# Performance work log

Hardware: AMD Instinct MI355X
Metric: run time of the kernel (lower is better)

Reference implementation:

```python
import jax, jax.numpy as jnp
import numpy as np
from jax import lax

EPS = 1e-06


def setup_inputs() -> dict:
    key = jax.random.key(0)
    B, MICS, T, F = 16, 4, 2048, 257
    x = jax.random.uniform(key, (B, MICS, T, F), dtype=jnp.float32)
    s = jnp.array([0.025], dtype=jnp.float32)
    alpha = jnp.array([0.98], dtype=jnp.float32)
    delta = jnp.array([2.0], dtype=jnp.float32)
    r = jnp.array([0.5], dtype=jnp.float32)
    return {"x": x, "s": s, "alpha": alpha, "delta": delta, "r": r}


def reference(x, s, alpha, delta, r):
    # x: [batch, mics, chans, frames]; EMA recurrence runs over dim 2 (split dim -2 in source)
    B, MICS, T, F = x.shape
    xr = x.reshape(B * MICS, T, F)
    xt = jnp.moveaxis(xr, 1, 0)  # [T, BM, F] -- scan axis first

    s0 = s[0]

    def step(carry, frame):
        m = (1.0 - s0) * carry + s0 * frame
        return m, m

    m0 = xt[0]  # first frame: M_0 = x_0 (last_state=None branch)
    _, ms = lax.scan(step, m0, xt[1:])
    M = jnp.concatenate([m0[None], ms], axis=0)  # [T, BM, F]
    M = jnp.moveaxis(M, 0, 1)  # [BM, T, F]

    # pcen nonlinearity: (x / (M+eps)^alpha + delta)^r - delta^r
    out = jnp.power(xr / jnp.power(M + EPS, alpha) + delta, r) - jnp.power(delta, r)
    return out.reshape(B, MICS, T, F)
```

## Files before the change

kernel.cpp:

```cpp
#include <hip/hip_runtime.h>
#include <hip/hip_bf16.h>


#define EPS 1e-6f

constexpr int BM = 64;
constexpr int T  = 2048;
constexpr int F  = 257;
constexpr int L  = 32;
constexpr int C  = T / L;
constexpr int NBLK = BM * C;
constexpr size_t MLOC_BYTES = (size_t)BM * C * F * sizeof(float);

__device__ __forceinline__ float fast_exp2(float x) { return __builtin_amdgcn_exp2f(x); }
__device__ __forceinline__ float fast_log2(float x) { return __builtin_amdgcn_logf(x); }

__device__ __forceinline__ float pcen_nl(float xv, float m, float alpha,
                                         float delta, float r, float dr) {
  float inner = fmaf(xv, fast_exp2(-alpha * fast_log2(m + EPS)), delta);
  return fast_exp2(r * fast_log2(inner)) - dr;
}

__global__ __launch_bounds__(64, 4) void pcen_phase1(
    const float* __restrict__ x, const float* __restrict__ s_p,
    float* __restrict__ mloc) {
  const int b  = blockIdx.x;
  const int l  = threadIdx.x;
  const int bm = b >> 6;
  const int c  = b & (C - 1);

  const float s = s_p[0];
  const float a = 1.0f - s;

  const float* row = x + ((size_t)bm * T + (size_t)c * L) * F;

  float m0, m1, m2, m3, m4;
  if (c == 0) {
    m0 = row[l]; m1 = row[l + 64]; m2 = row[l + 128]; m3 = row[l + 192];
    m4 = row[256];
  } else {
    m0 = m1 = m2 = m3 = m4 = 0.0f;
  }

  const float* p = row;
  #pragma unroll 4
  for (int t = 0; t < L; ++t) {
    float x0 = p[l];
    float x1 = p[l + 64];
    float x2 = p[l + 128];
    float x3 = p[l + 192];
    float x4 = p[256];
    m0 = fmaf(a, m0, s * x0);
    m1 = fmaf(a, m1, s * x1);
    m2 = fmaf(a, m2, s * x2);
    m3 = fmaf(a, m3, s * x3);
    m4 = fmaf(a, m4, s * x4);
    p += F;
  }

  float* mp = mloc + ((size_t)bm * C + c) * F;
  mp[l] = m0; mp[l + 64] = m1; mp[l + 128] = m2; mp[l + 192] = m3;
  if (l == 0) mp[256] = m4;
}

__global__ __launch_bounds__(64, 4) void pcen_phase2(
    const float* __restrict__ x, const float* __restrict__ s_p,
    const float* __restrict__ alpha_p, const float* __restrict__ delta_p,
    const float* __restrict__ r_p, const float* __restrict__ mloc,
    float* __restrict__ out) {
  const int b  = blockIdx.x;
  const int l  = threadIdx.x;
  const int bm = b >> 6;
  const int c  = b & (C - 1);

  const float s     = s_p[0];
  const float a     = 1.0f - s;
  const float alpha = alpha_p[0];
  const float delta = delta_p[0];
  const float r     = r_p[0];
  const float dr    = fast_exp2(r * fast_log2(delta));

  float aL = a;
  #pragma unroll
  for (int i = 0; i < 5; ++i) aL *= aL;

  const size_t rowoff = ((size_t)bm * T + (size_t)c * L) * F;
  const float* row  = x + rowoff;
  float*       orow = out + rowoff;

  float m0, m1, m2, m3, m4;
  if (c == 0) {
    m0 = row[l]; m1 = row[l + 64]; m2 = row[l + 128]; m3 = row[l + 192];
    m4 = row[256];
  } else {
    const float* mp = mloc + (size_t)bm * C * F;
    m0 = mp[l]; m1 = mp[l + 64]; m2 = mp[l + 128]; m3 = mp[l + 192];
    m4 = mp[256];
    const float* q = mp + F;
    #pragma unroll 2
    for (int cc = 1; cc < c; ++cc) {
      m0 = fmaf(aL, m0, q[l]);
      m1 = fmaf(aL, m1, q[l + 64]);
      m2 = fmaf(aL, m2, q[l + 128]);
      m3 = fmaf(aL, m3, q[l + 192]);
      m4 = fmaf(aL, m4, q[256]);
      q += F;
    }
  }

  const float* p  = row;
  float*       op = orow;
  #pragma unroll 2
  for (int t = 0; t < L; ++t) {
    float x0 = p[l];
    float x1 = p[l + 64];
    float x2 = p[l + 128];
    float x3 = p[l + 192];
    float x4 = p[256];
    m0 = fmaf(a, m0, s * x0);
    m1 = fmaf(a, m1, s * x1);
    m2 = fmaf(a, m2, s * x2);
    m3 = fmaf(a, m3, s * x3);
    m4 = fmaf(a, m4, s * x4);
    __builtin_nontemporal_store(pcen_nl(x0, m0, alpha, delta, r, dr), &op[l]);
    __builtin_nontemporal_store(pcen_nl(x1, m1, alpha, delta, r, dr), &op[l + 64]);
    __builtin_nontemporal_store(pcen_nl(x2, m2, alpha, delta, r, dr), &op[l + 128]);
    __builtin_nontemporal_store(pcen_nl(x3, m3, alpha, delta, r, dr), &op[l + 192]);
    if (l == 0)
      __builtin_nontemporal_store(pcen_nl(x4, m4, alpha, delta, r, dr), &op[256]);
    p  += F;
    op += F;
  }
}

constexpr int FB_L = 128;
constexpr int FB_C = T / FB_L;
constexpr int FB_H = 256;
__global__ __launch_bounds__(64, 4) void pcen_fallback(
    const float* __restrict__ x, const float* __restrict__ s_p,
    const float* __restrict__ alpha_p, const float* __restrict__ delta_p,
    const float* __restrict__ r_p, float* __restrict__ out) {
  const int b  = blockIdx.x;
  const int l  = threadIdx.x;
  const int bm = b / FB_C;
  const int c  = b % FB_C;

  const float s     = s_p[0];
  const float a     = 1.0f - s;
  const float alpha = alpha_p[0];
  const float delta = delta_p[0];
  const float r     = r_p[0];
  const float dr    = fast_exp2(r * fast_log2(delta));

  const size_t colbase = (size_t)bm * T * F;
  const int tstart = c * FB_L;
  int t0 = tstart - FB_H; if (t0 < 0) t0 = 0;

  float m0, m1, m2, m3, m4;
  const float* row0 = x + colbase + (size_t)t0 * F;
  if (t0 == 0) {
    m0 = row0[l]; m1 = row0[l + 64]; m2 = row0[l + 128]; m3 = row0[l + 192];
    m4 = row0[256];
  } else {
    m0 = m1 = m2 = m3 = m4 = 0.0f;
  }

  const float* p = row0;
  for (int t = t0; t < tstart; ++t) {
    float x0 = p[l], x1 = p[l + 64], x2 = p[l + 128], x3 = p[l + 192], x4 = p[256];
    m0 = fmaf(a, m0, s * x0); m1 = fmaf(a, m1, s * x1);
    m2 = fmaf(a, m2, s * x2); m3 = fmaf(a, m3, s * x3);
    m4 = fmaf(a, m4, s * x4);
    p += F;
  }
  p = x + colbase + (size_t)tstart * F;
  float* op = out + colbase + (size_t)tstart * F;
  for (int t = 0; t < FB_L; ++t) {
    float x0 = p[l], x1 = p[l + 64], x2 = p[l + 128], x3 = p[l + 192], x4 = p[256];
    m0 = fmaf(a, m0, s * x0); m1 = fmaf(a, m1, s * x1);
    m2 = fmaf(a, m2, s * x2); m3 = fmaf(a, m3, s * x3);
    m4 = fmaf(a, m4, s * x4);
    __builtin_nontemporal_store(pcen_nl(x0, m0, alpha, delta, r, dr), &op[l]);
    __builtin_nontemporal_store(pcen_nl(x1, m1, alpha, delta, r, dr), &op[l + 64]);
    __builtin_nontemporal_store(pcen_nl(x2, m2, alpha, delta, r, dr), &op[l + 128]);
    __builtin_nontemporal_store(pcen_nl(x3, m3, alpha, delta, r, dr), &op[l + 192]);
    if (l == 0)
      __builtin_nontemporal_store(pcen_nl(x4, m4, alpha, delta, r, dr), &op[256]);
    p  += F;
    op += F;
  }
}

extern "C" void kernel_launch(void* const* d_in, const int* in_sizes, int n_in,
                              void* d_out, int out_size, void* d_ws, size_t ws_size,
                              hipStream_t stream) {
  const float* x     = (const float*)d_in[0];
  const float* s     = (const float*)d_in[1];
  const float* alpha = (const float*)d_in[2];
  const float* delta = (const float*)d_in[3];
  const float* r     = (const float*)d_in[4];
  float* out = (float*)d_out;

  if (d_ws != nullptr && ws_size >= MLOC_BYTES) {
    float* mloc = (float*)d_ws;
    pcen_phase1<<<NBLK, 64, 0, stream>>>(x, s, mloc);
    pcen_phase2<<<NBLK, 64, 0, stream>>>(x, s, alpha, delta, r, mloc, out);
  } else {
    pcen_fallback<<<BM * FB_C, 64, 0, stream>>>(x, s, alpha, delta, r, out);
  }
}
```

Measured before the change: 301.0 us.

## Stage time tiles through double-buffered LDS with float4 loads, larger chunks

Both phases now use 256-thread blocks that copy contiguous 16-frame tiles of x into a double-buffered shared-memory buffer with coalesced float4 loads, then run the per-column EMA scan from LDS. Each thread owns one frequency column instead of five, and the chunk length grows from 32 to 128 frames, so there are fewer chunks and a shorter carry-prefix loop in phase 2. The goal is to replace strided scalar global loads with wide contiguous loads and overlap prefetch with compute. In exchange there are fewer blocks (1024), a barrier per tile, and a serial column 256 handled by a single thread.

```diff
diff --git a/kernel.cpp b/kernel.cpp
--- a/kernel.cpp
+++ b/kernel.cpp
@@ -1,5 +1,4 @@
 #include <hip/hip_runtime.h>
-#include <hip/hip_bf16.h>
 
 
 #define EPS 1e-6f
@@ -7,9 +6,12 @@
 constexpr int BM = 64;
 constexpr int T  = 2048;
 constexpr int F  = 257;
-constexpr int L  = 32;
+constexpr int L  = 128;
 constexpr int C  = T / L;
-constexpr int NBLK = BM * C;
+constexpr int TF = 16;
+constexpr int NT = L / TF;
+constexpr int NQ = TF * F / 4;
+constexpr int BLKS = BM * C;
 constexpr size_t MLOC_BYTES = (size_t)BM * C * F * sizeof(float);
 
 __device__ __forceinline__ float fast_exp2(float x) { return __builtin_amdgcn_exp2f(x); }
@@ -21,57 +23,81 @@
   return fast_exp2(r * fast_log2(inner)) - dr;
 }
 
-__global__ __launch_bounds__(64, 4) void pcen_phase1(
+__global__ __launch_bounds__(256, 4) void pcen_phase1(
     const float* __restrict__ x, const float* __restrict__ s_p,
     float* __restrict__ mloc) {
-  const int b  = blockIdx.x;
-  const int l  = threadIdx.x;
-  const int bm = b >> 6;
-  const int c  = b & (C - 1);
+  __shared__ float4 sb[2][NQ];
+  const int tid = threadIdx.x;
+  const int bm  = blockIdx.x >> 4;
+  const int c   = blockIdx.x & (C - 1);
 
   const float s = s_p[0];
   const float a = 1.0f - s;
 
-  const float* row = x + ((size_t)bm * T + (size_t)c * L) * F;
-
-  float m0, m1, m2, m3, m4;
-  if (c == 0) {
-    m0 = row[l]; m1 = row[l + 64]; m2 = row[l + 128]; m3 = row[l + 192];
-    m4 = row[256];
-  } else {
-    m0 = m1 = m2 = m3 = m4 = 0.0f;
-  }
-
-  const float* p = row;
-  #pragma unroll 4
-  for (int t = 0; t < L; ++t) {
-    float x0 = p[l];
-    float x1 = p[l + 64];
-    float x2 = p[l + 128];
-    float x3 = p[l + 192];
-    float x4 = p[256];
-    m0 = fmaf(a, m0, s * x0);
-    m1 = fmaf(a, m1, s * x1);
-    m2 = fmaf(a, m2, s * x2);
-    m3 = fmaf(a, m3, s * x3);
-    m4 = fmaf(a, m4, s * x4);
-    p += F;
-  }
-
-  float* mp = mloc + ((size_t)bm * C + c) * F;
-  mp[l] = m0; mp[l + 64] = m1; mp[l + 128] = m2; mp[l + 192] = m3;
-  if (l == 0) mp[256] = m4;
-}
-
-__global__ __launch_bounds__(64, 4) void pcen_phase2(
+  const float* xb = x + (size_t)(bm * T + c * L) * F;
+  const float4* src = reinterpret_cast<const float4*>(xb);
+
+  {
+    float4 v0 = src[tid], v1 = src[256 + tid], v2 = src[512 + tid], v3 = src[768 + tid];
+    float4 vt = make_float4(0.f, 0.f, 0.f, 0.f);
+    if (tid < 4) vt = src[1024 + tid];
+    float4* dst = sb[0];
+    dst[tid] = v0; dst[256 + tid] = v1; dst[512 + tid] = v2; dst[768 + tid] = v3;
+    if (tid < 4) dst[1024 + tid] = vt;
+  }
+  __syncthreads();
+
+  float m, mt = 0.0f;
+  {
+    const float* l0 = reinterpret_cast<const float*>(sb[0]);
+    if (c == 0) {
+      m = l0[tid];
+      if (tid == 0) mt = l0[256];
+    } else {
+      m = 0.0f;
+    }
+  }
+
+  for (int tt = 0; tt < NT; ++tt) {
+    const float* lp = reinterpret_cast<const float*>(sb[tt & 1]);
+    const bool more = (tt + 1 < NT);
+    float4 v0, v1, v2, v3, vt = make_float4(0.f, 0.f, 0.f, 0.f);
+    if (more) {
+      const float4* s2 = src + (size_t)(tt + 1) * NQ;
+      v0 = s2[tid]; v1 = s2[256 + tid]; v2 = s2[512 + tid]; v3 = s2[768 + tid];
+      if (tid < 4) vt = s2[1024 + tid];
+    }
+    #pragma unroll
+    for (int t = 0; t < TF; ++t) {
+      float xv = lp[t * F + tid];
+      m = fmaf(a, m, s * xv);
+    }
+    if (tid == 0) {
+      #pragma unroll
+      for (int t = 0; t < TF; ++t) mt = fmaf(a, mt, s * lp[t * F + 256]);
+    }
+    if (more) {
+      float4* dst = sb[(tt & 1) ^ 1];
+      dst[tid] = v0; dst[256 + tid] = v1; dst[512 + tid] = v2; dst[768 + tid] = v3;
+      if (tid < 4) dst[1024 + tid] = vt;
+    }
+    __syncthreads();
+  }
+
+  float* mp = mloc + (size_t)(bm * C + c) * F;
+  mp[tid] = m;
+  if (tid == 0) mp[256] = mt;
+}
+
+__global__ __launch_bounds__(256, 4) void pcen_phase2(
     const float* __restrict__ x, const float* __restrict__ s_p,
     const float* __restrict__ alpha_p, const float* __restrict__ delta_p,
     const float* __restrict__ r_p, const float* __restrict__ mloc,
     float* __restrict__ out) {
-  const int b  = blockIdx.x;
-  const int l  = threadIdx.x;
-  const int bm = b >> 6;
-  const int c  = b & (C - 1);
+  __shared__ float4 sb[2][NQ];
+  const int tid = threadIdx.x;
+  const int bm  = blockIdx.x >> 4;
+  const int c   = blockIdx.x & (C - 1);
 
   const float s     = s_p[0];
   const float a     = 1.0f - s;
@@ -82,54 +108,73 @@
 
   float aL = a;
   #pragma unroll
-  for (int i = 0; i < 5; ++i) aL *= aL;
-
-  const size_t rowoff = ((size_t)bm * T + (size_t)c * L) * F;
-  const float* row  = x + rowoff;
-  float*       orow = out + rowoff;
-
-  float m0, m1, m2, m3, m4;
+  for (int i = 0; i < 7; ++i) aL *= aL;
+
+  const size_t rowoff = (size_t)(bm * T + c * L) * F;
+  const float* xb = x + rowoff;
+  float*       ob = out + rowoff;
+  const float4* src = reinterpret_cast<const float4*>(xb);
+
+  float m = 0.0f, mt = 0.0f;
+  if (c > 0) {
+    const float* mp = mloc + (size_t)bm * C * F;
+    m = mp[tid];
+    if (tid == 0) mt = mp[256];
+    #pragma unroll 4
+    for (int cc = 1; cc < c; ++cc) {
+      m = fmaf(aL, m, mp[cc * F + tid]);
+      if (tid == 0) mt = fmaf(aL, mt, mp[cc * F + 256]);
+    }
+  }
+
+  {
+    float4 v0 = src[tid], v1 = src[256 + tid], v2 = src[512 + tid], v3 = src[768 + tid];
+    float4 vt = make_float4(0.f, 0.f, 0.f, 0.f);
+    if (tid < 4) vt = src[1024 + tid];
+    float4* dst = sb[0];
+    dst[tid] = v0; dst[256 + tid] = v1; dst[512 + tid] = v2; dst[768 + tid] = v3;
+    if (tid < 4) dst[1024 + tid] = vt;
+  }
+  __syncthreads();
+
   if (c == 0) {
-    m0 = row[l]; m1 = row[l + 64]; m2 = row[l + 128]; m3 = row[l + 192];
-    m4 = row[256];
-  } else {
-    const float* mp = mloc + (size_t)bm * C * F;
-    m0 = mp[l]; m1 = mp[l + 64]; m2 = mp[l + 128]; m3 = mp[l + 192];
-    m4 = mp[256];
-    const float* q = mp + F;
-    #pragma unroll 2
-    for (int cc = 1; cc < c; ++cc) {
-      m0 = fmaf(aL, m0, q[l]);
-      m1 = fmaf(aL, m1, q[l + 64]);
-      m2 = fmaf(aL, m2, q[l + 128]);
-      m3 = fmaf(aL, m3, q[l + 192]);
-      m4 = fmaf(aL, m4, q[256]);
-      q += F;
-    }
-  }
-
-  const float* p  = row;
-  float*       op = orow;
-  #pragma unroll 2
-  for (int t = 0; t < L; ++t) {
-    float x0 = p[l];
-    float x1 = p[l + 64];
-    float x2 = p[l + 128];
-    float x3 = p[l + 192];
-    float x4 = p[256];
-    m0 = fmaf(a, m0, s * x0);
-    m1 = fmaf(a, m1, s * x1);
-    m2 = fmaf(a, m2, s * x2);
-    m3 = fmaf(a, m3, s * x3);
-    m4 = fmaf(a, m4, s * x4);
-    __builtin_nontemporal_store(pcen_nl(x0, m0, alpha, delta, r, dr), &op[l]);
-    __builtin_nontemporal_store(pcen_nl(x1, m1, alpha, delta, r, dr), &op[l + 64]);
-    __builtin_nontemporal_store(pcen_nl(x2, m2, alpha, delta, r, dr), &op[l + 128]);
-    __builtin_nontemporal_store(pcen_nl(x3, m3, alpha, delta, r, dr), &op[l + 192]);
-    if (l == 0)
-      __builtin_nontemporal_store(pcen_nl(x4, m4, alpha, delta, r, dr), &op[256]);
-    p  += F;
-    op += F;
+    const float* l0 = reinterpret_cast<const float*>(sb[0]);
+    m = l0[tid];
+    mt = (tid == 0) ? l0[256] : 0.0f;
+  }
+
+  for (int tt = 0; tt < NT; ++tt) {
+    const float* lp = reinterpret_cast<const float*>(sb[tt & 1]);
+    float* op = ob + (size_t)tt * TF * F;
+    const bool more = (tt + 1 < NT);
+    float4 v0, v1, v2, v3, vt = make_float4(0.f, 0.f, 0.f, 0.f);
+    if (more) {
+      const float4* s2 = src + (size_t)(tt + 1) * NQ;
+      v0 = s2[tid]; v1 = s2[256 + tid]; v2 = s2[512 + tid]; v3 = s2[768 + tid];
+      if (tid < 4) vt = s2[1024 + tid];
+    }
+    #pragma unroll
+    for (int t = 0; t < TF; ++t) {
+      float xv = lp[t * F + tid];
+      m = fmaf(a, m, s * xv);
+      __builtin_nontemporal_store(pcen_nl(xv, m, alpha, delta, r, dr),
+                                  &op[t * F + tid]);
+    }
+    if (tid == 0) {
+      #pragma unroll
+      for (int t = 0; t < TF; ++t) {
+        float xv = lp[t * F + 256];
+        mt = fmaf(a, mt, s * xv);
+        __builtin_nontemporal_store(pcen_nl(xv, mt, alpha, delta, r, dr),
+                                    &op[t * F + 256]);
+      }
+    }
+    if (more) {
+      float4* dst = sb[(tt & 1) ^ 1];
+      dst[tid] = v0; dst[256 + tid] = v1; dst[512 + tid] = v2; dst[768 + tid] = v3;
+      if (tid < 4) dst[1024 + tid] = vt;
+    }
+    __syncthreads();
   }
 }
 
@@ -203,8 +248,8 @@
 
   if (d_ws != nullptr && ws_size >= MLOC_BYTES) {
     float* mloc = (float*)d_ws;
-    pcen_phase1<<<NBLK, 64, 0, stream>>>(x, s, mloc);
-    pcen_phase2<<<NBLK, 64, 0, stream>>>(x, s, alpha, delta, r, mloc, out);
+    pcen_phase1<<<BLKS, 256, 0, stream>>>(x, s, mloc);
+    pcen_phase2<<<BLKS, 256, 0, stream>>>(x, s, alpha, delta, r, mloc, out);
   } else {
     pcen_fallback<<<BM * FB_C, 64, 0, stream>>>(x, s, alpha, delta, r, out);
   }
```

After: 291.2 us. -3.2%, faster.
